# Performance work log

Hardware: AMD Instinct MI355X
Metric: run time of the kernel (lower is better)

## Reference

```python
import jax, jax.numpy as jnp
import numpy as np

N_EMBD = 768
N_HEAD = 12
B, T = 2, 2048
EPS = 1e-5


def _layernorm(x, g, b):
    mu = jnp.mean(x, axis=-1, keepdims=True)
    var = jnp.var(x, axis=-1, keepdims=True)
    return (x - mu) * jax.lax.rsqrt(var + EPS) * g + b


def _mha(q, k, v, causal):
    # q,k,v: [B,T,C] already projected
    Bq, Tq, C = q.shape
    d = C // N_HEAD
    q = q.reshape(Bq, Tq, N_HEAD, d).transpose(0, 2, 1, 3)  # b h t d
    k = k.reshape(Bq, Tq, N_HEAD, d).transpose(0, 2, 1, 3)
    v = v.reshape(Bq, Tq, N_HEAD, d).transpose(0, 2, 1, 3)
    scores = jnp.einsum('bhqd,bhkd->bhqk', q, k) * (1.0 / jnp.sqrt(jnp.float32(d)))
    if causal:
        mask = jnp.tril(jnp.ones((Tq, Tq), dtype=bool))
        scores = jnp.where(mask[None, None], scores, jnp.float32(-jnp.inf))
    att = jax.nn.softmax(scores, axis=-1)
    y = jnp.einsum('bhqk,bhkd->bhqd', att, v)
    return y.transpose(0, 2, 1, 3).reshape(Bq, Tq, C)


def setup_inputs() -> dict:
    key = jax.random.key(0)
    ks = iter(jax.random.split(key, 32))
    C = N_EMBD

    def lin(kk, din, dout):
        w = jax.random.normal(kk, (din, dout), jnp.float32) * (1.0 / np.sqrt(din))
        return w

    inp = {
        'x': jax.random.normal(next(ks), (B, T, C), jnp.float32),
        'encoder_output': jax.random.normal(next(ks), (B, T, C), jnp.float32),
        'ln1_g': jnp.ones((C,), jnp.float32), 'ln1_b': jnp.zeros((C,), jnp.float32),
        'attn_qkv_w': lin(next(ks), C, 3 * C), 'attn_qkv_b': jnp.zeros((3 * C,), jnp.float32),
        'attn_proj_w': lin(next(ks), C, C), 'attn_proj_b': jnp.zeros((C,), jnp.float32),
        'ln2_g': jnp.ones((C,), jnp.float32), 'ln2_b': jnp.zeros((C,), jnp.float32),
        'ca_q_w': lin(next(ks), C, C), 'ca_q_b': jnp.zeros((C,), jnp.float32),
        'ca_k_w': lin(next(ks), C, C), 'ca_k_b': jnp.zeros((C,), jnp.float32),
        'ca_v_w': lin(next(ks), C, C), 'ca_v_b': jnp.zeros((C,), jnp.float32),
        'ca_o_w': lin(next(ks), C, C), 'ca_o_b': jnp.zeros((C,), jnp.float32),
        'ln3_g': jnp.ones((C,), jnp.float32), 'ln3_b': jnp.zeros((C,), jnp.float32),
        'fc_w': lin(next(ks), C, 4 * C), 'fc_b': jnp.zeros((4 * C,), jnp.float32),
        'fc2_w': lin(next(ks), 4 * C, C), 'fc2_b': jnp.zeros((C,), jnp.float32),
    }
    return inp


def reference(x, encoder_output, ln1_g, ln1_b, attn_qkv_w, attn_qkv_b,
              attn_proj_w, attn_proj_b, ln2_g, ln2_b,
              ca_q_w, ca_q_b, ca_k_w, ca_k_b, ca_v_w, ca_v_b, ca_o_w, ca_o_b,
              ln3_g, ln3_b, fc_w, fc_b, fc2_w, fc2_b):
    C = N_EMBD
    # causal self-attention
    qkv = x @ attn_qkv_w + attn_qkv_b
    q, k, v = qkv[..., :C], qkv[..., C:2 * C], qkv[..., 2 * C:]
    sa = _mha(q, k, v, causal=True) @ attn_proj_w + attn_proj_b
    x = _layernorm(sa + x, ln1_g, ln1_b)
    # cross-attention
    cq = x @ ca_q_w + ca_q_b
    ck = encoder_output @ ca_k_w + ca_k_b
    cv = encoder_output @ ca_v_w + ca_v_b
    ca = _mha(cq, ck, cv, causal=False) @ ca_o_w + ca_o_b
    x = _layernorm(ca + x, ln2_g, ln2_b)
    # MLP
    h = jax.nn.relu(x @ fc_w + fc_b) @ fc2_w + fc2_b
    x = _layernorm(h + x, ln3_g, ln3_b)
    return x
```

## Files before the change

kernel.cpp:

```cpp
#include <hip/hip_runtime.h>


#define C_EMBD 768
#define NHEAD  12
#define HD     64
#define TB     2048
#define BB     2
#define MTOK   (BB*TB)

typedef __bf16 bf16_8 __attribute__((ext_vector_type(8)));
typedef float  f32x4  __attribute__((ext_vector_type(4)));

#define EXP2(x) exp2f(x)

__device__ __forceinline__ unsigned short f2bf(float f) {
    union { __bf16 h; unsigned short u; } c;
    c.h = (__bf16)f;
    return c.u;
}

#define GLOAD_LDS16(gsrc, ldst) \
    __builtin_amdgcn_global_load_lds( \
        (const __attribute__((address_space(1))) void*)(gsrc), \
        (__attribute__((address_space(3))) void*)(ldst), 16, 0, 0)

__global__ __launch_bounds__(256) void k_preproc(
        const float* __restrict__ x,     const float* __restrict__ enc,
        const float* __restrict__ qkv_w, const float* __restrict__ proj_w,
        const float* __restrict__ caq_w, const float* __restrict__ cak_w,
        const float* __restrict__ cav_w, const float* __restrict__ cao_w,
        const float* __restrict__ fc_w,  const float* __restrict__ fc2_w,
        const float* __restrict__ qkv_b, const float* __restrict__ caq_b,
        const float* __restrict__ cak_b, const float* __restrict__ cav_b,
        unsigned short* __restrict__ xbf,  unsigned short* __restrict__ encbf,
        unsigned short* __restrict__ wqkv, unsigned short* __restrict__ wproj,
        unsigned short* __restrict__ wcq,  unsigned short* __restrict__ wck,
        unsigned short* __restrict__ wcv,  unsigned short* __restrict__ wco,
        unsigned short* __restrict__ wfc,  unsigned short* __restrict__ wfc2,
        float* __restrict__ bqkv, float* __restrict__ bkv, float* __restrict__ bcq,
        float sc2) {
    __shared__ float tile[32][33];
    int b = blockIdx.x, tid = threadIdx.x;
    if (b < 9216) {
        const float* W; unsigned short* Wt; int K, N, t; float sc; int slim;
        if      (b < 1728) { W=qkv_w;  Wt=wqkv;  K=768;  N=2304; t=b;      sc=sc2; slim=768; }
        else if (b < 2304) { W=proj_w; Wt=wproj; K=768;  N=768;  t=b-1728; sc=1.f; slim=0;   }
        else if (b < 2880) { W=caq_w;  Wt=wcq;   K=768;  N=768;  t=b-2304; sc=sc2; slim=768; }
        else if (b < 3456) { W=cak_w;  Wt=wck;   K=768;  N=768;  t=b-2880; sc=1.f; slim=0;   }
        else if (b < 4032) { W=cav_w;  Wt=wcv;   K=768;  N=768;  t=b-3456; sc=1.f; slim=0;   }
        else if (b < 4608) { W=cao_w;  Wt=wco;   K=768;  N=768;  t=b-4032; sc=1.f; slim=0;   }
        else if (b < 6912) { W=fc_w;   Wt=wfc;   K=768;  N=3072; t=b-4608; sc=1.f; slim=0;   }
        else               { W=fc2_w;  Wt=wfc2;  K=3072; N=768;  t=b-6912; sc=1.f; slim=0;   }
        int ntx = N >> 5;
        int n0 = (t % ntx) * 32, k0 = (t / ntx) * 32;
        int tx = tid & 31, ty = tid >> 5;
#pragma unroll
        for (int i = 0; i < 4; ++i)
            tile[ty + 8*i][tx] = W[(size_t)(k0 + ty + 8*i) * N + n0 + tx];
        __syncthreads();
#pragma unroll
        for (int i = 0; i < 4; ++i) {
            int nrow = n0 + ty + 8*i;
            float s = (nrow < slim) ? sc : 1.0f;
            Wt[(size_t)nrow * K + k0 + tx] = f2bf(tile[tx][ty + 8*i] * s);
        }
    } else if (b < 15360) {
        int b2 = b - 9216;
        const float* src = (b2 < 3072) ? x   : enc;
        unsigned short* dst = (b2 < 3072) ? xbf : encbf;
        int i = (b2 < 3072 ? b2 : b2 - 3072) * 256 + tid;
        float4 v = ((const float4*)src)[i];
        ushort4 o;
        o.x = f2bf(v.x); o.y = f2bf(v.y); o.z = f2bf(v.z); o.w = f2bf(v.w);
        ((ushort4*)dst)[i] = o;
    } else {
        int b3 = b - 15360;
        if (b3 < 9) {
            int i = b3 * 256 + tid;
            if (i < 2304) bqkv[i] = qkv_b[i] * (i < 768 ? sc2 : 1.0f);
        } else if (b3 < 12) {
            int i = (b3 - 9) * 256 + tid;
            if (i < 768) { bkv[i] = cak_b[i]; bkv[768 + i] = cav_b[i]; }
        } else {
            int i = (b3 - 12) * 256 + tid;
            if (i < 768) bcq[i] = caq_b[i] * sc2;
        }
    }
}

template<int BM, bool OUT_BF16, bool ADD_RES, bool RELU>
__global__ __launch_bounds__(256) void k_gemm_bt(
        const unsigned short* __restrict__ A,
        const unsigned short* __restrict__ Bt,
        const float* __restrict__ bias,
        const float* __restrict__ res,
        void* __restrict__ Cout,
        int M, int N, int K) {
    constexpr int MF = BM / 32;
    __shared__ unsigned short As[BM * 32];
    __shared__ unsigned short Bs[128 * 32];
    int tid  = threadIdx.x;
    int lane = tid & 63, wave = tid >> 6;
    int l16 = lane & 15, lg = lane >> 4;
    int wm = (wave >> 1) * (BM / 2), wn = (wave & 1) * 64;
    int bm = blockIdx.x * BM, bn = blockIdx.y * 128;

    f32x4 acc[MF][4] = {};

    for (int k0 = 0; k0 < K; k0 += 32) {
        __syncthreads();
#pragma unroll
        for (int i = 0; i < BM / 64; ++i) {
            int chunk = i * 256 + tid;
            GLOAD_LDS16(A + (size_t)(bm + (chunk >> 2)) * K + k0 + (chunk & 3) * 8,
                        As + (size_t)(i * 256 + wave * 64) * 8);
        }
#pragma unroll
        for (int i = 0; i < 2; ++i) {
            int chunk = i * 256 + tid;
            GLOAD_LDS16(Bt + (size_t)(bn + (chunk >> 2)) * K + k0 + (chunk & 3) * 8,
                        Bs + (size_t)(i * 256 + wave * 64) * 8);
        }
        __syncthreads();
        bf16_8 af[MF], bfr[4];
#pragma unroll
        for (int m = 0; m < MF; ++m)
            af[m]  = *(const bf16_8*)(As + (size_t)(wm + m*16 + l16) * 32 + lg * 8);
#pragma unroll
        for (int n = 0; n < 4; ++n)
            bfr[n] = *(const bf16_8*)(Bs + (size_t)(wn + n*16 + l16) * 32 + lg * 8);
#pragma unroll
        for (int m = 0; m < MF; ++m)
#pragma unroll
            for (int n = 0; n < 4; ++n)
                acc[m][n] = __builtin_amdgcn_mfma_f32_16x16x32_bf16(af[m], bfr[n], acc[m][n], 0, 0, 0);
    }

#pragma unroll
    for (int m = 0; m < MF; ++m) {
#pragma unroll
        for (int n = 0; n < 4; ++n) {
            int col = bn + wn + n*16 + l16;
            float bv = bias[col];
#pragma unroll
            for (int r = 0; r < 4; ++r) {
                int row = bm + wm + m*16 + lg*4 + r;
                float v = acc[m][n][r] + bv;
                if (ADD_RES) v += res[(size_t)row * N + col];
                if (RELU)    v = fmaxf(v, 0.f);
                if (OUT_BF16) ((unsigned short*)Cout)[(size_t)row * N + col] = f2bf(v);
                else          ((float*)Cout)[(size_t)row * N + col] = v;
            }
        }
    }
}

template<bool CAUSAL>
__global__ __launch_bounds__(256) void k_attn(
        const unsigned short* __restrict__ Qp,
        const unsigned short* __restrict__ Kp,
        const unsigned short* __restrict__ Vp,
        unsigned short* __restrict__ Yp,
        int strideQ, int strideKV) {
    __shared__ __bf16 Ks[64][72];
    __shared__ __bf16 Vt[64][72];
    __shared__ __bf16 Ps[4][16][72];
    int tid  = threadIdx.x;
    int lane = tid & 63, wave = tid >> 6;
    int l16 = lane & 15, lg = lane >> 4;
    int bh = blockIdx.y;
    int b = bh / NHEAD, h = bh - b * NHEAD;

    const unsigned short* Qb = Qp + (size_t)b * TB * strideQ  + h * HD;
    const unsigned short* Kb = Kp + (size_t)b * TB * strideKV + h * HD;
    const unsigned short* Vb = Vp + (size_t)b * TB * strideKV + h * HD;

    bf16_8 vones;
#pragma unroll
    for (int j = 0; j < 8; ++j) vones[j] = (__bf16)1.0f;

    int kr = tid >> 3, kc = (tid & 7) * 8;
    int vk2 = (tid & 31) * 2;
    int vd0 = (tid >> 5) * 8;
    const size_t stepKV = (size_t)64 * strideKV;

    const int npass = CAUSAL ? 2 : 1;
    for (int pass = 0; pass < npass; ++pass) {
        int qt = CAUSAL ? (pass == 0 ? (TB/64 - 1 - (int)blockIdx.x) : (int)blockIdx.x)
                        : (int)blockIdx.x;
        int wq = qt * 64 + wave * 16;

        bf16_8 qf0 = *(const bf16_8*)(Qb + (size_t)(wq + l16) * strideQ + lg * 8);
        bf16_8 qf1 = *(const bf16_8*)(Qb + (size_t)(wq + l16) * strideQ + 32 + lg * 8);

        const unsigned short* gK0 = Kb + (size_t)kr  * strideKV + kc;
        const unsigned short* gK1 = gK0 + (size_t)32 * strideKV;
        const unsigned short* gV0 = Vb + (size_t)vk2 * strideKV + vd0;
        const unsigned short* gV1 = gV0 + strideKV;

        int4 kA = *(const int4*)gK0;
        int4 kB = *(const int4*)gK1;
        unsigned vp[8];
        {
            int4 va = *(const int4*)gV0, vb2 = *(const int4*)gV1;
            const unsigned short* pa = (const unsigned short*)&va;
            const unsigned short* pb = (const unsigned short*)&vb2;
#pragma unroll
            for (int j = 0; j < 8; ++j) vp[j] = (unsigned)pa[j] | ((unsigned)pb[j] << 16);
        }

        f32x4 o[4] = {};
        float m_run[4], l_run[4];
#pragma unroll
        for (int r = 0; r < 4; ++r) { m_run[r] = -1e30f; l_run[r] = 0.f; }

        int ktEnd = CAUSAL ? (qt + 1) : (TB / 64);
        for (int kt = 0; kt < ktEnd; ++kt) {
            __syncthreads();
            *(int4*)(&Ks[kr][kc])      = kA;
            *(int4*)(&Ks[kr + 32][kc]) = kB;
#pragma unroll
            for (int j = 0; j < 8; ++j)
                *(unsigned*)(&Vt[vd0 + j][vk2]) = vp[j];
            __syncthreads();

            if (kt + 1 < ktEnd) {
                gK0 += stepKV; gK1 += stepKV; gV0 += stepKV; gV1 += stepKV;
                kA = *(const int4*)gK0;
                kB = *(const int4*)gK1;
                int4 va = *(const int4*)gV0, vb2 = *(const int4*)gV1;
                const unsigned short* pa = (const unsigned short*)&va;
                const unsigned short* pb = (const unsigned short*)&vb2;
#pragma unroll
                for (int j = 0; j < 8; ++j) vp[j] = (unsigned)pa[j] | ((unsigned)pb[j] << 16);
            }

            f32x4 s[4];
#pragma unroll
            for (int n = 0; n < 4; ++n) {
                f32x4 z = {};
                bf16_8 kf0 = *(const bf16_8*)(&Ks[n*16 + l16][lg*8]);
                bf16_8 kf1 = *(const bf16_8*)(&Ks[n*16 + l16][32 + lg*8]);
                z = __builtin_amdgcn_mfma_f32_16x16x32_bf16(qf0, kf0, z, 0, 0, 0);
                z = __builtin_amdgcn_mfma_f32_16x16x32_bf16(qf1, kf1, z, 0, 0, 0);
                s[n] = z;
            }
            if (CAUSAL && kt == qt) {
#pragma unroll
                for (int n = 0; n < 4; ++n)
#pragma unroll
                    for (int r = 0; r < 4; ++r)
                        if (kt*64 + n*16 + l16 > wq + lg*4 + r) s[n][r] = -1e30f;
            }
            float mx[4];
#pragma unroll
            for (int r = 0; r < 4; ++r)
                mx[r] = fmaxf(fmaxf(s[0][r], s[1][r]), fmaxf(s[2][r], s[3][r]));
#pragma unroll
            for (int off = 1; off < 16; off <<= 1)
#pragma unroll
                for (int r = 0; r < 4; ++r)
                    mx[r] = fmaxf(mx[r], __shfl_xor(mx[r], off, 64));
            bool big = (mx[0] > m_run[0] + 8.f) | (mx[1] > m_run[1] + 8.f) |
                       (mx[2] > m_run[2] + 8.f) | (mx[3] > m_run[3] + 8.f);
            if (__any(big)) {
#pragma unroll
                for (int r = 0; r < 4; ++r) {
                    float mnew = fmaxf(m_run[r], mx[r]);
                    float sf = EXP2(m_run[r] - mnew);
                    m_run[r] = mnew;
                    l_run[r] *= sf;
#pragma unroll
                    for (int n = 0; n < 4; ++n) o[n][r] *= sf;
                }
            }
#pragma unroll
            for (int n = 0; n < 4; ++n)
#pragma unroll
                for (int r = 0; r < 4; ++r)
                    Ps[wave][lg*4 + r][n*16 + l16] = (__bf16)EXP2(s[n][r] - m_run[r]);

            f32x4 zsum = {};
#pragma unroll
            for (int kk = 0; kk < 2; ++kk) {
                bf16_8 pa = *(const bf16_8*)(&Ps[wave][l16][kk*32 + lg*8]);
                zsum = __builtin_amdgcn_mfma_f32_16x16x32_bf16(pa, vones, zsum, 0, 0, 0);
#pragma unroll
                for (int n = 0; n < 4; ++n) {
                    bf16_8 vf = *(const bf16_8*)(&Vt[n*16 + l16][kk*32 + lg*8]);
                    o[n] = __builtin_amdgcn_mfma_f32_16x16x32_bf16(pa, vf, o[n], 0, 0, 0);
                }
            }
#pragma unroll
            for (int r = 0; r < 4; ++r) l_run[r] += zsum[r];
        }

#pragma unroll
        for (int r = 0; r < 4; ++r) {
            float rl = 1.0f / l_run[r];
            int token = b * TB + wq + lg*4 + r;
#pragma unroll
            for (int n = 0; n < 4; ++n)
                Yp[(size_t)token * C_EMBD + h * HD + n*16 + l16] = f2bf(o[n][r] * rl);
        }
    }
}

template<bool WF32, bool WBF16>
__global__ __launch_bounds__(256) void k_ln(const float* __restrict__ in,
                                            const float* __restrict__ g,
                                            const float* __restrict__ bb,
                                            float* __restrict__ outf,
                                            unsigned short* __restrict__ outb) {
    int row = blockIdx.x;
    const float* x = in + (size_t)row * C_EMBD;
    float v[3], s1 = 0.f, s2 = 0.f;
#pragma unroll
    for (int i = 0; i < 3; ++i) {
        v[i] = x[threadIdx.x + i * 256];
        s1 += v[i];
        s2 += v[i] * v[i];
    }
#pragma unroll
    for (int off = 1; off < 64; off <<= 1) {
        s1 += __shfl_xor(s1, off, 64);
        s2 += __shfl_xor(s2, off, 64);
    }
    __shared__ float red[8];
    int wave = threadIdx.x >> 6, lane = threadIdx.x & 63;
    if (lane == 0) { red[wave] = s1; red[4 + wave] = s2; }
    __syncthreads();
    s1 = red[0] + red[1] + red[2] + red[3];
    s2 = red[4] + red[5] + red[6] + red[7];
    float mu  = s1 * (1.f / C_EMBD);
    float var = s2 * (1.f / C_EMBD) - mu * mu;
    float rs  = rsqrtf(var + 1e-5f);
#pragma unroll
    for (int i = 0; i < 3; ++i) {
        int c = threadIdx.x + i * 256;
        float y = (v[i] - mu) * rs * g[c] + bb[c];
        if (WF32)  outf[(size_t)row * C_EMBD + c] = y;
        if (WBF16) outb[(size_t)row * C_EMBD + c] = f2bf(y);
    }
}

extern "C" void kernel_launch(void* const* d_in, const int* in_sizes, int n_in,
                              void* d_out, int out_size, void* d_ws, size_t ws_size,
                              hipStream_t stream) {
    (void)in_sizes; (void)n_in; (void)out_size; (void)ws_size;
    const float* x      = (const float*)d_in[0];
    const float* enc    = (const float*)d_in[1];
    const float* ln1_g  = (const float*)d_in[2];
    const float* ln1_b  = (const float*)d_in[3];
    const float* qkv_w  = (const float*)d_in[4];
    const float* qkv_b  = (const float*)d_in[5];
    const float* proj_w = (const float*)d_in[6];
    const float* proj_b = (const float*)d_in[7];
    const float* ln2_g  = (const float*)d_in[8];
    const float* ln2_b  = (const float*)d_in[9];
    const float* caq_w  = (const float*)d_in[10];
    const float* caq_b  = (const float*)d_in[11];
    const float* cak_w  = (const float*)d_in[12];
    const float* cak_b  = (const float*)d_in[13];
    const float* cav_w  = (const float*)d_in[14];
    const float* cav_b  = (const float*)d_in[15];
    const float* cao_w  = (const float*)d_in[16];
    const float* cao_b  = (const float*)d_in[17];
    const float* ln3_g  = (const float*)d_in[18];
    const float* ln3_b  = (const float*)d_in[19];
    const float* fc_w   = (const float*)d_in[20];
    const float* fc_b   = (const float*)d_in[21];
    const float* fc2_w  = (const float*)d_in[22];
    const float* fc2_b  = (const float*)d_in[23];
    float* out = (float*)d_out;

    char* ws = (char*)d_ws;
    auto us = [&](size_t off) { return (unsigned short*)(ws + off); };
    auto fl = [&](size_t off) { return (float*)(ws + off); };

    const size_t O_WQKV  = 0;
    const size_t O_WPROJ = 3538944;
    const size_t O_WCQ   = 4718592;
    const size_t O_WCK   = 5898240;
    const size_t O_WCV   = 7077888;
    const size_t O_WCO   = 8257536;
    const size_t O_WFC   = 9437184;
    const size_t O_WFC2  = 14155776;
    const size_t O_XBF   = 18874368;
    const size_t O_ENCBF = 25165824;
    const size_t O_QKVBF = 31457280;
    const size_t O_Q2    = O_QKVBF;
    const size_t O_KV2   = O_QKVBF + 6291456;
    const size_t O_YBF   = 50331648;
    const size_t O_RESF  = 56623104;
    const size_t O_X1F   = 69206016;
    const size_t O_X1BF  = 81788928;
    const size_t O_X2F   = 88080384;
    const size_t O_X2BF  = 100663296;
    const size_t O_HBF   = 106954752;
    const size_t O_BKV   = O_HBF;
    const size_t O_BQKV  = O_HBF + 8192;
    const size_t O_BCQ   = O_HBF + 20480;

    const float SC2 = 0.125f * 1.44269504f;

    k_preproc<<<15375, 256, 0, stream>>>(
        x, enc, qkv_w, proj_w, caq_w, cak_w, cav_w, cao_w, fc_w, fc2_w,
        qkv_b, caq_b, cak_b, cav_b,
        us(O_XBF), us(O_ENCBF),
        us(O_WQKV), us(O_WPROJ), us(O_WCQ), us(O_WCK),
        us(O_WCV), us(O_WCO), us(O_WFC), us(O_WFC2),
        fl(O_BQKV), fl(O_BKV), fl(O_BCQ), SC2);

    k_gemm_bt<128, true,  false, false><<<dim3(32, 18), 256, 0, stream>>>(
        us(O_XBF), us(O_WQKV), fl(O_BQKV), nullptr, us(O_QKVBF), MTOK, 2304, 768);
    k_attn<true><<<dim3(TB/128, BB*NHEAD), 256, 0, stream>>>(
        us(O_QKVBF), us(O_QKVBF) + 768, us(O_QKVBF) + 1536, us(O_YBF), 2304, 2304);
    k_gemm_bt<64, false, true,  false><<<dim3(64, 6), 256, 0, stream>>>(
        us(O_YBF), us(O_WPROJ), proj_b, x, fl(O_RESF), MTOK, 768, 768);
    k_ln<true, true><<<MTOK, 256, 0, stream>>>(fl(O_RESF), ln1_g, ln1_b, fl(O_X1F), us(O_X1BF));
    k_gemm_bt<64, true,  false, false><<<dim3(64, 6), 256, 0, stream>>>(
        us(O_X1BF),  us(O_WCQ), fl(O_BCQ), nullptr, us(O_Q2), MTOK, 768, 768);
    k_gemm_bt<128, true,  false, false><<<dim3(32, 12), 256, 0, stream>>>(
        us(O_ENCBF), us(O_WCK), fl(O_BKV), nullptr, us(O_KV2), MTOK, 1536, 768);
    k_attn<false><<<dim3(TB/64, BB*NHEAD), 256, 0, stream>>>(
        us(O_Q2), us(O_KV2), us(O_KV2) + 768, us(O_YBF), 768, 1536);
    k_gemm_bt<64, false, true,  false><<<dim3(64, 6), 256, 0, stream>>>(
        us(O_YBF), us(O_WCO), cao_b, fl(O_X1F), fl(O_RESF), MTOK, 768, 768);
    k_ln<true, true><<<MTOK, 256, 0, stream>>>(fl(O_RESF), ln2_g, ln2_b, fl(O_X2F), us(O_X2BF));
    k_gemm_bt<128, true,  false, true ><<<dim3(32, 24), 256, 0, stream>>>(
        us(O_X2BF), us(O_WFC), fc_b, nullptr, us(O_HBF), MTOK, 3072, 768);
    k_gemm_bt<64, false, true,  false><<<dim3(64, 6), 256, 0, stream>>>(
        us(O_HBF), us(O_WFC2), fc2_b, fl(O_X2F), fl(O_RESF), MTOK, 768, 3072);
    k_ln<true, false><<<MTOK, 256, 0, stream>>>(fl(O_RESF), ln3_g, ln3_b, out, nullptr);
}
```

Baseline: 496.8 us.

## Double-buffer attention K/V tiles and launch one causal query tile per block

The attention kernel now keeps two LDS buffers for K and V. The next tile is written into the alternate buffer after the current tile's compute, which cuts the barriers per iteration from two to one. The causal launch drops the two-pass pairing of a long and a short query tile per block and uses one tile per block on a doubled grid, with heavy tiles scheduled first. EXP2 also switches to the hardware exp2 builtin; in exchange, LDS use doubles for K/V and per-block work becomes unbalanced in the causal case.

```diff
diff --git a/kernel.cpp b/kernel.cpp
--- a/kernel.cpp
+++ b/kernel.cpp
@@ -11,7 +11,11 @@
 typedef __bf16 bf16_8 __attribute__((ext_vector_type(8)));
 typedef float  f32x4  __attribute__((ext_vector_type(4)));
 
+#if __has_builtin(__builtin_amdgcn_exp2f)
+#define EXP2(x) __builtin_amdgcn_exp2f(x)
+#else
 #define EXP2(x) exp2f(x)
+#endif
 
 __device__ __forceinline__ unsigned short f2bf(float f) {
     union { __bf16 h; unsigned short u; } c;
@@ -162,18 +166,23 @@
         const unsigned short* __restrict__ Vp,
         unsigned short* __restrict__ Yp,
         int strideQ, int strideKV) {
-    __shared__ __bf16 Ks[64][72];
-    __shared__ __bf16 Vt[64][72];
+    __shared__ __bf16 Ks[2][64][72];
+    __shared__ __bf16 Vt[2][64][72];
     __shared__ __bf16 Ps[4][16][72];
     int tid  = threadIdx.x;
     int lane = tid & 63, wave = tid >> 6;
     int l16 = lane & 15, lg = lane >> 4;
     int bh = blockIdx.y;
     int b = bh / NHEAD, h = bh - b * NHEAD;
+    int qt = CAUSAL ? (gridDim.x - 1 - blockIdx.x) : blockIdx.x;
+    int wq = qt * 64 + wave * 16;
 
     const unsigned short* Qb = Qp + (size_t)b * TB * strideQ  + h * HD;
     const unsigned short* Kb = Kp + (size_t)b * TB * strideKV + h * HD;
     const unsigned short* Vb = Vp + (size_t)b * TB * strideKV + h * HD;
+
+    bf16_8 qf0 = *(const bf16_8*)(Qb + (size_t)(wq + l16) * strideQ + lg * 8);
+    bf16_8 qf1 = *(const bf16_8*)(Qb + (size_t)(wq + l16) * strideQ + 32 + lg * 8);
 
     bf16_8 vones;
 #pragma unroll
@@ -184,24 +193,41 @@
     int vd0 = (tid >> 5) * 8;
     const size_t stepKV = (size_t)64 * strideKV;
 
-    const int npass = CAUSAL ? 2 : 1;
-    for (int pass = 0; pass < npass; ++pass) {
-        int qt = CAUSAL ? (pass == 0 ? (TB/64 - 1 - (int)blockIdx.x) : (int)blockIdx.x)
-                        : (int)blockIdx.x;
-        int wq = qt * 64 + wave * 16;
-
-        bf16_8 qf0 = *(const bf16_8*)(Qb + (size_t)(wq + l16) * strideQ + lg * 8);
-        bf16_8 qf1 = *(const bf16_8*)(Qb + (size_t)(wq + l16) * strideQ + 32 + lg * 8);
-
-        const unsigned short* gK0 = Kb + (size_t)kr  * strideKV + kc;
-        const unsigned short* gK1 = gK0 + (size_t)32 * strideKV;
-        const unsigned short* gV0 = Vb + (size_t)vk2 * strideKV + vd0;
-        const unsigned short* gV1 = gV0 + strideKV;
-
-        int4 kA = *(const int4*)gK0;
-        int4 kB = *(const int4*)gK1;
-        unsigned vp[8];
-        {
+    const unsigned short* gK0 = Kb + (size_t)kr  * strideKV + kc;
+    const unsigned short* gK1 = gK0 + (size_t)32 * strideKV;
+    const unsigned short* gV0 = Vb + (size_t)vk2 * strideKV + vd0;
+    const unsigned short* gV1 = gV0 + strideKV;
+
+    int4 kA = *(const int4*)gK0;
+    int4 kB = *(const int4*)gK1;
+    unsigned vp[8];
+    {
+        int4 va = *(const int4*)gV0, vb2 = *(const int4*)gV1;
+        const unsigned short* pa = (const unsigned short*)&va;
+        const unsigned short* pb = (const unsigned short*)&vb2;
+#pragma unroll
+        for (int j = 0; j < 8; ++j) vp[j] = (unsigned)pa[j] | ((unsigned)pb[j] << 16);
+    }
+    *(int4*)(&Ks[0][kr][kc])      = kA;
+    *(int4*)(&Ks[0][kr + 32][kc]) = kB;
+#pragma unroll
+    for (int j = 0; j < 8; ++j)
+        *(unsigned*)(&Vt[0][vd0 + j][vk2]) = vp[j];
+    __syncthreads();
+
+    f32x4 o[4] = {};
+    float m_run[4], l_run[4];
+#pragma unroll
+    for (int r = 0; r < 4; ++r) { m_run[r] = -1e30f; l_run[r] = 0.f; }
+
+    int ktEnd = CAUSAL ? (qt + 1) : (TB / 64);
+    for (int kt = 0; kt < ktEnd; ++kt) {
+        int cur = kt & 1;
+        bool more = (kt + 1 < ktEnd);
+        if (more) {
+            gK0 += stepKV; gK1 += stepKV; gV0 += stepKV; gV1 += stepKV;
+            kA = *(const int4*)gK0;
+            kB = *(const int4*)gK1;
             int4 va = *(const int4*)gV0, vb2 = *(const int4*)gV1;
             const unsigned short* pa = (const unsigned short*)&va;
             const unsigned short* pb = (const unsigned short*)&vb2;
@@ -209,100 +235,82 @@
             for (int j = 0; j < 8; ++j) vp[j] = (unsigned)pa[j] | ((unsigned)pb[j] << 16);
         }
 
-        f32x4 o[4] = {};
-        float m_run[4], l_run[4];
-#pragma unroll
-        for (int r = 0; r < 4; ++r) { m_run[r] = -1e30f; l_run[r] = 0.f; }
-
-        int ktEnd = CAUSAL ? (qt + 1) : (TB / 64);
-        for (int kt = 0; kt < ktEnd; ++kt) {
-            __syncthreads();
-            *(int4*)(&Ks[kr][kc])      = kA;
-            *(int4*)(&Ks[kr + 32][kc]) = kB;
+        f32x4 s[4];
+#pragma unroll
+        for (int n = 0; n < 4; ++n) {
+            f32x4 z = {};
+            bf16_8 kf0 = *(const bf16_8*)(&Ks[cur][n*16 + l16][lg*8]);
+            bf16_8 kf1 = *(const bf16_8*)(&Ks[cur][n*16 + l16][32 + lg*8]);
+            z = __builtin_amdgcn_mfma_f32_16x16x32_bf16(qf0, kf0, z, 0, 0, 0);
+            z = __builtin_amdgcn_mfma_f32_16x16x32_bf16(qf1, kf1, z, 0, 0, 0);
+            s[n] = z;
+        }
+        if (CAUSAL && kt == qt) {
+#pragma unroll
+            for (int n = 0; n < 4; ++n)
+#pragma unroll
+                for (int r = 0; r < 4; ++r)
+                    if (kt*64 + n*16 + l16 > wq + lg*4 + r) s[n][r] = -1e30f;
+        }
+        float mx[4];
+#pragma unroll
+        for (int r = 0; r < 4; ++r)
+            mx[r] = fmaxf(fmaxf(s[0][r], s[1][r]), fmaxf(s[2][r], s[3][r]));
+#pragma unroll
+        for (int off = 1; off < 16; off <<= 1)
+#pragma unroll
+            for (int r = 0; r < 4; ++r)
+                mx[r] = fmaxf(mx[r], __shfl_xor(mx[r], off, 64));
+        bool big = (mx[0] > m_run[0] + 8.f) | (mx[1] > m_run[1] + 8.f) |
+                   (mx[2] > m_run[2] + 8.f) | (mx[3] > m_run[3] + 8.f);
+        if (__any(big)) {
+#pragma unroll
+            for (int r = 0; r < 4; ++r) {
+                float mnew = fmaxf(m_run[r], mx[r]);
+                float sf = EXP2(m_run[r] - mnew);
+                m_run[r] = mnew;
+                l_run[r] *= sf;
+#pragma unroll
+                for (int n = 0; n < 4; ++n) o[n][r] *= sf;
+            }
+        }
+#pragma unroll
+        for (int n = 0; n < 4; ++n)
+#pragma unroll
+            for (int r = 0; r < 4; ++r)
+                Ps[wave][lg*4 + r][n*16 + l16] = (__bf16)EXP2(s[n][r] - m_run[r]);
+
+        f32x4 zsum = {};
+#pragma unroll
+        for (int kk = 0; kk < 2; ++kk) {
+            bf16_8 pa = *(const bf16_8*)(&Ps[wave][l16][kk*32 + lg*8]);
+            zsum = __builtin_amdgcn_mfma_f32_16x16x32_bf16(pa, vones, zsum, 0, 0, 0);
+#pragma unroll
+            for (int n = 0; n < 4; ++n) {
+                bf16_8 vf = *(const bf16_8*)(&Vt[cur][n*16 + l16][kk*32 + lg*8]);
+                o[n] = __builtin_amdgcn_mfma_f32_16x16x32_bf16(pa, vf, o[n], 0, 0, 0);
+            }
+        }
+#pragma unroll
+        for (int r = 0; r < 4; ++r) l_run[r] += zsum[r];
+
+        if (more) {
+            *(int4*)(&Ks[cur ^ 1][kr][kc])      = kA;
+            *(int4*)(&Ks[cur ^ 1][kr + 32][kc]) = kB;
 #pragma unroll
             for (int j = 0; j < 8; ++j)
-                *(unsigned*)(&Vt[vd0 + j][vk2]) = vp[j];
-            __syncthreads();
-
-            if (kt + 1 < ktEnd) {
-                gK0 += stepKV; gK1 += stepKV; gV0 += stepKV; gV1 += stepKV;
-                kA = *(const int4*)gK0;
-                kB = *(const int4*)gK1;
-                int4 va = *(const int4*)gV0, vb2 = *(const int4*)gV1;
-                const unsigned short* pa = (const unsigned short*)&va;
-                const unsigned short* pb = (const unsigned short*)&vb2;
-#pragma unroll
-                for (int j = 0; j < 8; ++j) vp[j] = (unsigned)pa[j] | ((unsigned)pb[j] << 16);
-            }
-
-            f32x4 s[4];
-#pragma unroll
-            for (int n = 0; n < 4; ++n) {
-                f32x4 z = {};
-                bf16_8 kf0 = *(const bf16_8*)(&Ks[n*16 + l16][lg*8]);
-                bf16_8 kf1 = *(const bf16_8*)(&Ks[n*16 + l16][32 + lg*8]);
-                z = __builtin_amdgcn_mfma_f32_16x16x32_bf16(qf0, kf0, z, 0, 0, 0);
-                z = __builtin_amdgcn_mfma_f32_16x16x32_bf16(qf1, kf1, z, 0, 0, 0);
-                s[n] = z;
-            }
-            if (CAUSAL && kt == qt) {
-#pragma unroll
-                for (int n = 0; n < 4; ++n)
-#pragma unroll
-                    for (int r = 0; r < 4; ++r)
-                        if (kt*64 + n*16 + l16 > wq + lg*4 + r) s[n][r] = -1e30f;
-            }
-            float mx[4];
-#pragma unroll
-            for (int r = 0; r < 4; ++r)
-                mx[r] = fmaxf(fmaxf(s[0][r], s[1][r]), fmaxf(s[2][r], s[3][r]));
-#pragma unroll
-            for (int off = 1; off < 16; off <<= 1)
-#pragma unroll
-                for (int r = 0; r < 4; ++r)
-                    mx[r] = fmaxf(mx[r], __shfl_xor(mx[r], off, 64));
-            bool big = (mx[0] > m_run[0] + 8.f) | (mx[1] > m_run[1] + 8.f) |
-                       (mx[2] > m_run[2] + 8.f) | (mx[3] > m_run[3] + 8.f);
-            if (__any(big)) {
-#pragma unroll
-                for (int r = 0; r < 4; ++r) {
-                    float mnew = fmaxf(m_run[r], mx[r]);
-                    float sf = EXP2(m_run[r] - mnew);
-                    m_run[r] = mnew;
-                    l_run[r] *= sf;
-#pragma unroll
-                    for (int n = 0; n < 4; ++n) o[n][r] *= sf;
-                }
-            }
-#pragma unroll
-            for (int n = 0; n < 4; ++n)
-#pragma unroll
-                for (int r = 0; r < 4; ++r)
-                    Ps[wave][lg*4 + r][n*16 + l16] = (__bf16)EXP2(s[n][r] - m_run[r]);
-
-            f32x4 zsum = {};
-#pragma unroll
-            for (int kk = 0; kk < 2; ++kk) {
-                bf16_8 pa = *(const bf16_8*)(&Ps[wave][l16][kk*32 + lg*8]);
-                zsum = __builtin_amdgcn_mfma_f32_16x16x32_bf16(pa, vones, zsum, 0, 0, 0);
-#pragma unroll
-                for (int n = 0; n < 4; ++n) {
-                    bf16_8 vf = *(const bf16_8*)(&Vt[n*16 + l16][kk*32 + lg*8]);
-                    o[n] = __builtin_amdgcn_mfma_f32_16x16x32_bf16(pa, vf, o[n], 0, 0, 0);
-                }
-            }
-#pragma unroll
-            for (int r = 0; r < 4; ++r) l_run[r] += zsum[r];
-        }
-
-#pragma unroll
-        for (int r = 0; r < 4; ++r) {
-            float rl = 1.0f / l_run[r];
-            int token = b * TB + wq + lg*4 + r;
-#pragma unroll
-            for (int n = 0; n < 4; ++n)
-                Yp[(size_t)token * C_EMBD + h * HD + n*16 + l16] = f2bf(o[n][r] * rl);
-        }
+                *(unsigned*)(&Vt[cur ^ 1][vd0 + j][vk2]) = vp[j];
+        }
+        __syncthreads();
+    }
+
+#pragma unroll
+    for (int r = 0; r < 4; ++r) {
+        float rl = 1.0f / l_run[r];
+        int token = b * TB + wq + lg*4 + r;
+#pragma unroll
+        for (int n = 0; n < 4; ++n)
+            Yp[(size_t)token * C_EMBD + h * HD + n*16 + l16] = f2bf(o[n][r] * rl);
     }
 }
 
@@ -414,7 +422,7 @@
 
     k_gemm_bt<128, true,  false, false><<<dim3(32, 18), 256, 0, stream>>>(
         us(O_XBF), us(O_WQKV), fl(O_BQKV), nullptr, us(O_QKVBF), MTOK, 2304, 768);
-    k_attn<true><<<dim3(TB/128, BB*NHEAD), 256, 0, stream>>>(
+    k_attn<true><<<dim3(TB/64, BB*NHEAD), 256, 0, stream>>>(
         us(O_QKVBF), us(O_QKVBF) + 768, us(O_QKVBF) + 1536, us(O_YBF), 2304, 2304);
     k_gemm_bt<64, false, true,  false><<<dim3(64, 6), 256, 0, stream>>>(
         us(O_YBF), us(O_WPROJ), proj_b, x, fl(O_RESF), MTOK, 768, 768);
```

New measurement: 502.3 us. No clear change (+1.1%).
